# Kernel tuning notes

Measured on AMD Instinct MI355X. Metric: run time of the kernel, lower is better.

## Reference

```python
import jax, jax.numpy as jnp
import numpy as np

G = 8          # n_games
D_IN = 512     # per-game input dim (equal for all games)
H1 = 1024
H2 = 1024
A = 128        # max_actions
B = 8192       # batch rows


def setup_inputs() -> dict:
    key = jax.random.key(0)
    ks = jax.random.split(key, 9)
    state = jax.random.normal(ks[0], (B, D_IN), dtype=jnp.float32)
    idx = jax.random.randint(ks[1], (B,), 0, G, dtype=jnp.int32)
    # per-game input linears: uniform(-1/sqrt(fan_in), 1/sqrt(fan_in))
    lim1 = 1.0 / np.sqrt(D_IN)
    W1 = jax.random.uniform(ks[2], (G, D_IN, H1), minval=-lim1, maxval=lim1, dtype=jnp.float32)
    b1 = jax.random.uniform(ks[3], (G, H1), minval=-lim1, maxval=lim1, dtype=jnp.float32)
    # shared linear
    lim2 = 1.0 / np.sqrt(H1)
    W2 = jax.random.uniform(ks[4], (H1, H2), minval=-lim2, maxval=lim2, dtype=jnp.float32)
    b2 = jax.random.uniform(ks[5], (H2,), minval=-lim2, maxval=lim2, dtype=jnp.float32)
    # per-game output heads: uniform(-0.003, 0.003)
    W3 = jax.random.uniform(ks[6], (G, H2, A), minval=-0.003, maxval=0.003, dtype=jnp.float32)
    b3 = jax.random.uniform(ks[7], (G, A), minval=-0.003, maxval=0.003, dtype=jnp.float32)
    return {"state": state, "idx": idx, "W1": W1, "b1": b1, "W2": W2, "b2": b2, "W3": W3, "b3": b3}


def reference(state, idx, W1, b1, W2, b2, W3, b3):
    # Torch code concatenates per-game groups in sorted-unique-idx order,
    # i.e. a stable permutation of rows by idx; reproduce exactly.
    perm = jnp.argsort(idx, stable=True)          # [B]
    s = state[perm]                               # [B, D_IN]
    g = idx[perm]                                 # [B] game of each permuted row
    # routed first layer: compute all games then gather per-row game
    h1_all = jnp.einsum('bd,gdh->bgh', s, W1) + b1            # [B, G, H1]
    h1 = jax.nn.relu(jnp.take_along_axis(h1_all, g[:, None, None], axis=1)[:, 0, :])  # [B, H1]
    h_f = jax.nn.relu(h1 @ W2 + b2)                            # [B, H2]
    a = jnp.tanh(jnp.einsum('bh,gha->bga', h_f, W3) + b3)      # [B, G, A]
    # NOTE: original gathers heads with the ORIGINAL (unpermuted) idx,
    # even though rows of `a` are in permuted order. Reproduce faithfully.
    out = jnp.take_along_axis(a, idx[:, None, None], axis=1)[:, 0, :]  # [B, A]
    return out
```

## Files before the change

kernel.cpp:

```cpp
#include <hip/hip_runtime.h>
#include <math.h>

#define G_GAMES 8
#define D_IN 512
#define H1 1024
#define H2 1024
#define A_DIM 128
#define B_ROWS 8192

typedef short bf16x8 __attribute__((ext_vector_type(8)));
typedef float f32x4 __attribute__((ext_vector_type(4)));

#define WS_OFF   0u
#define WS_PERM  256u
#define WS_SPERM 33280u
#define WS_W1T   (WS_SPERM + B_ROWS*D_IN*2u)
#define WS_W2T   (WS_W1T + G_GAMES*D_IN*H1*2u)
#define WS_W3T   (WS_W2T + (unsigned)H1*H2*2u)
#define WS_H1    (WS_W3T + G_GAMES*H2*A_DIM*2u)
#define WS_HF    WS_SPERM

__device__ __forceinline__ unsigned short f2bf(float x) {
  union { float f; unsigned int u; } v; v.f = x;
  unsigned int r = v.u + 0x7fffu + ((v.u >> 16) & 1u);
  return (unsigned short)(r >> 16);
}

__device__ __forceinline__ void async_load16(const void* gptr, void* ldsptr) {
  __builtin_amdgcn_global_load_lds(
      (const __attribute__((address_space(1))) unsigned int*)gptr,
      (__attribute__((address_space(3))) unsigned int*)ldsptr,
      16, 0, 0);
}

__device__ void sort_256(const int* __restrict__ idx, int* __restrict__ perm,
                         int* __restrict__ off) {
  __shared__ int wtot[4][9];
  __shared__ int wbase[4][9];
  __shared__ int offs[9];
  const int t = threadIdx.x, lane = t & 63, wave = t >> 6;
  int my[32];
#pragma unroll
  for (int i = 0; i < 8; ++i) {
    const int4 a = *(const int4*)(idx + t * 32 + i * 4);
    my[i*4+0] = a.x; my[i*4+1] = a.y; my[i*4+2] = a.z; my[i*4+3] = a.w;
  }
  int local[8] = {0,0,0,0,0,0,0,0};
#pragma unroll
  for (int i = 0; i < 32; ++i) local[my[i]]++;
  int incl[8];
#pragma unroll
  for (int g = 0; g < 8; ++g) {
    int v = local[g];
#pragma unroll
    for (int d = 1; d < 64; d <<= 1) {
      const int n = __shfl_up(v, d);
      if (lane >= d) v += n;
    }
    incl[g] = v;
  }
  if (lane == 63) {
#pragma unroll
    for (int g = 0; g < 8; ++g) wtot[wave][g] = incl[g];
  }
  __syncthreads();
  if (t < 8) {
    int s = 0;
#pragma unroll
    for (int w = 0; w < 4; ++w) { wbase[w][t] = s; s += wtot[w][t]; }
    wtot[0][t] = s;
  }
  __syncthreads();
  if (t == 0) {
    int s = 0;
#pragma unroll
    for (int g = 0; g < 8; ++g) { offs[g] = s; off[g] = s; s += wtot[0][g]; }
    offs[8] = s; off[8] = s;
  }
  __syncthreads();
  int start[8];
#pragma unroll
  for (int g = 0; g < 8; ++g)
    start[g] = offs[g] + wbase[wave][g] + (incl[g] - local[g]);
#pragma unroll
  for (int i = 0; i < 32; ++i) {
    const int g = my[i];
    perm[start[g]++] = t * 32 + i;
  }
}

__device__ void trans_tile(const float* __restrict__ in,
                           unsigned short* __restrict__ out,
                           int R, int C, int xt, int yt, int z) {
  in  += (size_t)z * R * C;
  out += (size_t)z * R * C;
  __shared__ float tile[64][65];
  const int c0 = xt * 64, r0 = yt * 64;
  const int tx = threadIdx.x & 63, ty = threadIdx.x >> 6;
#pragma unroll
  for (int rr = ty; rr < 64; rr += 4)
    tile[rr][tx] = in[(size_t)(r0 + rr) * C + c0 + tx];
  __syncthreads();
#pragma unroll
  for (int cc = ty; cc < 64; cc += 4)
    out[(size_t)(c0 + cc) * R + r0 + tx] = f2bf(tile[tx][cc]);
}

__global__ __launch_bounds__(256) void k_pre1(const float* __restrict__ W1,
                                              const float* __restrict__ W2,
                                              const float* __restrict__ W3,
                                              const int* __restrict__ idx,
                                              unsigned short* __restrict__ W1T,
                                              unsigned short* __restrict__ W2T,
                                              unsigned short* __restrict__ W3T,
                                              int* __restrict__ perm,
                                              int* __restrict__ off) {
  const int b = blockIdx.x;
  if (b < 1024) {
    const int z = b >> 7, r = b & 127;
    trans_tile(W1, W1T, D_IN, H1, r & 15, r >> 4, z);
  } else if (b < 1280) {
    const int r = b - 1024;
    trans_tile(W2, W2T, H1, H2, r & 15, r >> 4, 0);
  } else if (b < 1536) {
    const int r = (b - 1280) & 31, z = (b - 1280) >> 5;
    trans_tile(W3, W3T, H2, A_DIM, r & 1, r >> 1, z);
  } else {
    sort_256(idx, perm, off);
  }
}

__global__ __launch_bounds__(256) void k_gather(const float* __restrict__ state,
                                                const int* __restrict__ perm,
                                                unsigned short* __restrict__ sPerm) {
  const int p = blockIdx.x * 2 + (threadIdx.x >> 7);
  const int c = (threadIdx.x & 127) << 2;
  const int src = perm[p];
  const float4 v = *(const float4*)(state + (size_t)src * D_IN + c);
  ushort4 o;
  o.x = f2bf(v.x); o.y = f2bf(v.y); o.z = f2bf(v.z); o.w = f2bf(v.w);
  *(ushort4*)(sPerm + (size_t)p * D_IN + c) = o;
}

template <int KTOT>
__device__ __forceinline__ void gemm_db_core(const unsigned short* const* aP,
                                             const unsigned short* const* bP,
                                             char* smem, int tid, f32x4 acc[4][4]) {
  const int lane = tid & 63, wave = tid >> 6;
  const int wm = wave & 1, wn = wave >> 1;
  const int sw = lane & 15, quad = lane >> 4;
  const int mA = wm * 64 + sw;
  const int nB = wn * 64 + sw;
  char* A0 = smem;          char* A1 = smem + 16384;
  char* B0 = smem + 32768;  char* B1 = smem + 49152;
  const int NIT = KTOT >> 6;
#pragma unroll
  for (int c = 0; c < 4; ++c) {
    async_load16(aP[c], A0 + (wave * 32 + c * 8) * 128);
    async_load16(bP[c], B0 + (wave * 32 + c * 8) * 128);
  }
#pragma unroll 2
  for (int k = 0; k < NIT; ++k) {
    __syncthreads();
    char* A = (k & 1) ? A1 : A0;
    char* B = (k & 1) ? B1 : B0;
    if (k + 1 < NIT) {
      char* An = (k & 1) ? A0 : A1;
      char* Bn = (k & 1) ? B0 : B1;
      const int koff = (k + 1) << 6;
#pragma unroll
      for (int c = 0; c < 4; ++c) {
        async_load16(aP[c] + koff, An + (wave * 32 + c * 8) * 128);
        async_load16(bP[c] + koff, Bn + (wave * 32 + c * 8) * 128);
      }
    }
#pragma unroll
    for (int ks = 0; ks < 2; ++ks) {
      const int u = ((((ks << 2) + quad) ^ (sw & 7)) << 4);
      bf16x8 aF[4], bF[4];
#pragma unroll
      for (int i = 0; i < 4; ++i) {
        aF[i] = *(const bf16x8*)(A + (mA + i * 16) * 128 + u);
        bF[i] = *(const bf16x8*)(B + (nB + i * 16) * 128 + u);
      }
#pragma unroll
      for (int i = 0; i < 4; ++i)
#pragma unroll
        for (int j = 0; j < 4; ++j)
          acc[i][j] = __builtin_amdgcn_mfma_f32_16x16x32_bf16(aF[i], bF[j], acc[i][j], 0, 0, 0);
    }
  }
}

__device__ __forceinline__ bool seg_map(const int* __restrict__ off, int T,
                                        int& g, int& seg1, int& row0) {
  int base = 0;
  for (int gg = 0; gg < 8; ++gg) {
    const int s = off[gg], e = off[gg + 1];
    const int nt = (e - s + 127) >> 7;
    if (T < base + nt) { g = gg; seg1 = e; row0 = s + (T - base) * 128; return true; }
    base += nt;
  }
  return false;
}

__device__ __forceinline__ bool seg_map32(const int* __restrict__ off, int T,
                                          int& g, int& seg1, int& row0) {
  int base = 0;
  for (int gg = 0; gg < 8; ++gg) {
    const int s = off[gg], e = off[gg + 1];
    const int nt = (e - s + 31) >> 5;
    if (T < base + nt) { g = gg; seg1 = e; row0 = s + (T - base) * 32; return true; }
    base += nt;
  }
  return false;
}

__device__ __forceinline__ void epilogue_bf16(char* smem, const f32x4 acc[4][4],
                                              const float* bj, int tid,
                                              unsigned short* __restrict__ outp,
                                              size_t ldOut, int row0, int col0,
                                              int vrows) {
  const int lane = tid & 63, wave = tid >> 6;
  const int wm = wave & 1, wn = wave >> 1;
  const int sw = lane & 15, quad = lane >> 4;
  __syncthreads();
#pragma unroll
  for (int i = 0; i < 4; ++i)
#pragma unroll
    for (int j = 0; j < 4; ++j)
#pragma unroll
      for (int r = 0; r < 4; ++r) {
        const int row = wm * 64 + i * 16 + quad * 4 + r;
        const int col = wn * 64 + j * 16 + sw;
        const float v = fmaxf(acc[i][j][r] + bj[j], 0.0f);
        *(unsigned short*)(smem + row * 264 + col * 2) = f2bf(v);
      }
  __syncthreads();
#pragma unroll
  for (int q = 0; q < 8; ++q) {
    const int idxq = q * 256 + tid;
    const int row = idxq >> 4, ch = idxq & 15;
    if (row < vrows) {
      const uint2 lo = *(const uint2*)(smem + row * 264 + ch * 16);
      const uint2 hi = *(const uint2*)(smem + row * 264 + ch * 16 + 8);
      uint4 v; v.x = lo.x; v.y = lo.y; v.z = hi.x; v.w = hi.y;
      *(uint4*)((char*)outp + ((size_t)(row0 + row) * ldOut + col0 + ch * 8) * 2) = v;
    }
  }
}

__global__ __launch_bounds__(256) void k_gemm1(const unsigned short* __restrict__ sPerm,
                                               const unsigned short* __restrict__ W1T,
                                               const float* __restrict__ b1,
                                               const int* __restrict__ off,
                                               unsigned short* __restrict__ h1out) {
  __shared__ char smem[65536];
  int g, seg1, row0;
  if (!seg_map(off, blockIdx.x, g, seg1, row0)) return;
  const int col0 = blockIdx.y * 128;
  const int tid = threadIdx.x, lane = tid & 63, wave = tid >> 6;
  const int gcol = ((lane & 7) ^ (lane >> 3)) << 3;
  const unsigned short* aP[4];
  const unsigned short* bP[4];
#pragma unroll
  for (int c = 0; c < 4; ++c) {
    const int rl = wave * 32 + c * 8 + (lane >> 3);
    int p = row0 + rl;
    if (p > seg1 - 1) p = seg1 - 1;
    aP[c] = sPerm + (size_t)p * D_IN + gcol;
    bP[c] = W1T + (size_t)g * H1 * D_IN + (size_t)(col0 + rl) * D_IN + gcol;
  }
  f32x4 acc[4][4] = {};
  gemm_db_core<D_IN>(aP, bP, smem, tid, acc);
  const int wn = wave >> 1, sw = lane & 15;
  const float* bg = b1 + g * H1;
  float bj[4];
#pragma unroll
  for (int j = 0; j < 4; ++j) bj[j] = bg[col0 + wn * 64 + j * 16 + sw];
  const int vrows = min(128, seg1 - row0);
  epilogue_bf16(smem, acc, bj, tid, h1out, H1, row0, col0, vrows);
}

__global__ __launch_bounds__(256) void k_gemm2(const unsigned short* __restrict__ h1in,
                                               const unsigned short* __restrict__ W2T,
                                               const float* __restrict__ b2,
                                               unsigned short* __restrict__ hfout) {
  __shared__ char smem[65536];
  const int row0 = blockIdx.x * 128, col0 = blockIdx.y * 128;
  const int tid = threadIdx.x, lane = tid & 63, wave = tid >> 6;
  const int gcol = ((lane & 7) ^ (lane >> 3)) << 3;
  const unsigned short* aP[4];
  const unsigned short* bP[4];
#pragma unroll
  for (int c = 0; c < 4; ++c) {
    const int rl = wave * 32 + c * 8 + (lane >> 3);
    aP[c] = h1in + (size_t)(row0 + rl) * H1 + gcol;
    bP[c] = W2T + (size_t)(col0 + rl) * H1 + gcol;
  }
  f32x4 acc[4][4] = {};
  gemm_db_core<H1>(aP, bP, smem, tid, acc);
  const int wn = wave >> 1, sw = lane & 15;
  float bj[4];
#pragma unroll
  for (int j = 0; j < 4; ++j) bj[j] = b2[col0 + wn * 64 + j * 16 + sw];
  epilogue_bf16(smem, acc, bj, tid, hfout, H2, row0, col0, 128);
}

__global__ __launch_bounds__(256) void k_gemm3(const unsigned short* __restrict__ hf,
                                               const unsigned short* __restrict__ W3T,
                                               const float* __restrict__ b3,
                                               const int* __restrict__ off,
                                               const int* __restrict__ perm,
                                               float* __restrict__ outp) {
  __shared__ char smem[40960];
  int g, seg1, row0;
  if (!seg_map32(off, blockIdx.x, g, seg1, row0)) return;
  const int tid = threadIdx.x, lane = tid & 63, wave = tid >> 6;
  const int wm = wave & 1, wn = wave >> 1;
  const int sw = lane & 15, quad = lane >> 4;
  const int gcol = ((lane & 7) ^ (lane >> 3)) << 3;
  int q0 = row0 + wave * 8 + (lane >> 3);
  if (q0 > seg1 - 1) q0 = seg1 - 1;
  const unsigned short* aP = hf + (size_t)perm[q0] * H2 + gcol;
  const unsigned short* bP[4];
#pragma unroll
  for (int c = 0; c < 4; ++c) {
    const int rl = wave * 32 + c * 8 + (lane >> 3);
    bP[c] = W3T + (size_t)g * A_DIM * H2 + (size_t)rl * H2 + gcol;
  }
  char* A0 = smem;         char* A1 = smem + 4096;
  char* B0 = smem + 8192;  char* B1 = smem + 24576;
  const int mA = wm * 16 + sw;
  const int nB = wn * 64 + sw;
  f32x4 acc[4] = {};
  async_load16(aP, A0 + (wave * 8) * 128);
#pragma unroll
  for (int c = 0; c < 4; ++c)
    async_load16(bP[c], B0 + (wave * 32 + c * 8) * 128);
#pragma unroll 2
  for (int k = 0; k < (H2 >> 6); ++k) {
    __syncthreads();
    char* A = (k & 1) ? A1 : A0;
    char* B = (k & 1) ? B1 : B0;
    if (k + 1 < (H2 >> 6)) {
      char* An = (k & 1) ? A0 : A1;
      char* Bn = (k & 1) ? B0 : B1;
      const int koff = (k + 1) << 6;
      async_load16(aP + koff, An + (wave * 8) * 128);
#pragma unroll
      for (int c = 0; c < 4; ++c)
        async_load16(bP[c] + koff, Bn + (wave * 32 + c * 8) * 128);
    }
#pragma unroll
    for (int ks = 0; ks < 2; ++ks) {
      const int u = ((((ks << 2) + quad) ^ (sw & 7)) << 4);
      const bf16x8 aF = *(const bf16x8*)(A + mA * 128 + u);
      bf16x8 bF[4];
#pragma unroll
      for (int j = 0; j < 4; ++j)
        bF[j] = *(const bf16x8*)(B + (nB + j * 16) * 128 + u);
#pragma unroll
      for (int j = 0; j < 4; ++j)
        acc[j] = __builtin_amdgcn_mfma_f32_16x16x32_bf16(aF, bF[j], acc[j], 0, 0, 0);
    }
  }
  const float* bg = b3 + g * A_DIM;
  float bj[4];
#pragma unroll
  for (int j = 0; j < 4; ++j) bj[j] = bg[wn * 64 + j * 16 + sw];
  __syncthreads();
#pragma unroll
  for (int j = 0; j < 4; ++j)
#pragma unroll
    for (int r = 0; r < 4; ++r) {
      const int row = wm * 16 + quad * 4 + r;
      const int col = wn * 64 + j * 16 + sw;
      *(float*)(smem + row * 528 + col * 4) = tanhf(acc[j][r] + bj[j]);
    }
  __syncthreads();
#pragma unroll
  for (int qq = 0; qq < 4; ++qq) {
    const int idxq = qq * 256 + tid;
    const int row = idxq >> 5, ch = idxq & 31;
    if (row0 + row < seg1) {
      const uint4 v = *(const uint4*)(smem + row * 528 + ch * 16);
      *(uint4*)((char*)outp + ((size_t)perm[row0 + row] * A_DIM + ch * 4) * 4) = v;
    }
  }
}

extern "C" void kernel_launch(void* const* d_in, const int* in_sizes, int n_in,
                              void* d_out, int out_size, void* d_ws, size_t ws_size,
                              hipStream_t stream) {
  (void)in_sizes; (void)n_in; (void)out_size; (void)ws_size;
  const float* state = (const float*)d_in[0];
  const int*   idx   = (const int*)d_in[1];
  const float* W1    = (const float*)d_in[2];
  const float* b1    = (const float*)d_in[3];
  const float* W2    = (const float*)d_in[4];
  const float* b2    = (const float*)d_in[5];
  const float* W3    = (const float*)d_in[6];
  const float* b3    = (const float*)d_in[7];
  float* outp = (float*)d_out;
  char* ws = (char*)d_ws;
  int* off  = (int*)(ws + WS_OFF);
  int* perm = (int*)(ws + WS_PERM);
  unsigned short* sPerm = (unsigned short*)(ws + WS_SPERM);
  unsigned short* W1T   = (unsigned short*)(ws + WS_W1T);
  unsigned short* W2T   = (unsigned short*)(ws + WS_W2T);
  unsigned short* W3T   = (unsigned short*)(ws + WS_W3T);
  unsigned short* h1    = (unsigned short*)(ws + WS_H1);
  unsigned short* hf    = (unsigned short*)(ws + WS_HF);

  hipLaunchKernelGGL(k_pre1, dim3(1537), dim3(256), 0, stream,
                     W1, W2, W3, idx, W1T, W2T, W3T, perm, off);
  hipLaunchKernelGGL(k_gather, dim3(B_ROWS / 2), dim3(256), 0, stream, state, perm, sPerm);
  hipLaunchKernelGGL(k_gemm1, dim3(72, 8), dim3(256), 0, stream, sPerm, W1T, b1, off, h1);
  hipLaunchKernelGGL(k_gemm2, dim3(64, 8), dim3(256), 0, stream, h1, W2T, b2, hf);
  hipLaunchKernelGGL(k_gemm3, dim3(264), dim3(256), 0, stream, hf, W3T, b3, off, perm, outp);
}
```

Before: 156.3 us.

## Fuse state gather and bf16 conversion into gemm1, vectorize weight transpose

Removes the separate gather kernel. gemm1 now reads fp32 state rows through the permutation directly, converts them to bf16 in registers, and writes them into swizzled LDS. The weight-transpose tiles switch to float4 loads with packed bf16 conversion and 16-byte stores, which cuts global store transactions. In exchange, the A-operand loads become synchronous register loads instead of async LDS loads, and they read twice the bytes per element (fp32), which may reduce overlap inside gemm1.

```diff
diff --git a/kernel.cpp b/kernel.cpp
--- a/kernel.cpp
+++ b/kernel.cpp
@@ -26,6 +26,12 @@
   return (unsigned short)(r >> 16);
 }
 
+__device__ __forceinline__ unsigned int cvt_pk_bf16(float lo, float hi) {
+  unsigned int r;
+  asm("v_cvt_pk_bf16_f32 %0, %1, %2" : "=v"(r) : "v"(lo), "v"(hi));
+  return r;
+}
+
 __device__ __forceinline__ void async_load16(const void* gptr, void* ldsptr) {
   __builtin_amdgcn_global_load_lds(
       (const __attribute__((address_space(1))) unsigned int*)gptr,
@@ -94,16 +100,33 @@
                            int R, int C, int xt, int yt, int z) {
   in  += (size_t)z * R * C;
   out += (size_t)z * R * C;
-  __shared__ float tile[64][65];
+  __shared__ unsigned short tl[64][68];
   const int c0 = xt * 64, r0 = yt * 64;
-  const int tx = threadIdx.x & 63, ty = threadIdx.x >> 6;
-#pragma unroll
-  for (int rr = ty; rr < 64; rr += 4)
-    tile[rr][tx] = in[(size_t)(r0 + rr) * C + c0 + tx];
-  __syncthreads();
-#pragma unroll
-  for (int cc = ty; cc < 64; cc += 4)
-    out[(size_t)(c0 + cc) * R + r0 + tx] = f2bf(tile[tx][cc]);
+  const int t = threadIdx.x;
+#pragma unroll
+  for (int pass = 0; pass < 4; ++pass) {
+    const int id = pass * 256 + t;
+    const int r = id >> 4, f4c = (id & 15) << 2;
+    const float4 v = *(const float4*)(in + (size_t)(r0 + r) * C + c0 + f4c);
+    uint2 w;
+    w.x = cvt_pk_bf16(v.x, v.y);
+    w.y = cvt_pk_bf16(v.z, v.w);
+    *(uint2*)&tl[r][f4c] = w;
+  }
+  __syncthreads();
+#pragma unroll
+  for (int pass = 0; pass < 2; ++pass) {
+    const int cc = t >> 2, k0 = ((t & 3) << 3) + (pass << 5);
+    unsigned short u[8];
+#pragma unroll
+    for (int j = 0; j < 8; ++j) u[j] = tl[k0 + j][cc];
+    uint4 v;
+    v.x = (unsigned)u[0] | ((unsigned)u[1] << 16);
+    v.y = (unsigned)u[2] | ((unsigned)u[3] << 16);
+    v.z = (unsigned)u[4] | ((unsigned)u[5] << 16);
+    v.w = (unsigned)u[6] | ((unsigned)u[7] << 16);
+    *(uint4*)(out + (size_t)(c0 + cc) * R + r0 + k0) = v;
+  }
 }
 
 __global__ __launch_bounds__(256) void k_pre1(const float* __restrict__ W1,
@@ -130,18 +153,6 @@
   }
 }
 
-__global__ __launch_bounds__(256) void k_gather(const float* __restrict__ state,
-                                                const int* __restrict__ perm,
-                                                unsigned short* __restrict__ sPerm) {
-  const int p = blockIdx.x * 2 + (threadIdx.x >> 7);
-  const int c = (threadIdx.x & 127) << 2;
-  const int src = perm[p];
-  const float4 v = *(const float4*)(state + (size_t)src * D_IN + c);
-  ushort4 o;
-  o.x = f2bf(v.x); o.y = f2bf(v.y); o.z = f2bf(v.z); o.w = f2bf(v.w);
-  *(ushort4*)(sPerm + (size_t)p * D_IN + c) = o;
-}
-
 template <int KTOT>
 __device__ __forceinline__ void gemm_db_core(const unsigned short* const* aP,
                                              const unsigned short* const* bP,
@@ -250,30 +261,101 @@
   }
 }
 
-__global__ __launch_bounds__(256) void k_gemm1(const unsigned short* __restrict__ sPerm,
-                                               const unsigned short* __restrict__ W1T,
-                                               const float* __restrict__ b1,
-                                               const int* __restrict__ off,
-                                               unsigned short* __restrict__ h1out) {
-  __shared__ char smem[65536];
+__global__ __launch_bounds__(256, 2) void k_gemm1(const float* __restrict__ state,
+                                                  const int* __restrict__ perm,
+                                                  const unsigned short* __restrict__ W1T,
+                                                  const float* __restrict__ b1,
+                                                  const int* __restrict__ off,
+                                                  unsigned short* __restrict__ h1out) {
+  __shared__ __align__(16) char smem[65536];
   int g, seg1, row0;
   if (!seg_map(off, blockIdx.x, g, seg1, row0)) return;
   const int col0 = blockIdx.y * 128;
   const int tid = threadIdx.x, lane = tid & 63, wave = tid >> 6;
+  const int wm = wave & 1, wn = wave >> 1;
+  const int sw = lane & 15, quad = lane >> 4;
+  const int lc = lane & 7;
   const int gcol = ((lane & 7) ^ (lane >> 3)) << 3;
-  const unsigned short* aP[4];
+  const float* aS[4];
+  int ldsA[4];
   const unsigned short* bP[4];
 #pragma unroll
   for (int c = 0; c < 4; ++c) {
     const int rl = wave * 32 + c * 8 + (lane >> 3);
     int p = row0 + rl;
     if (p > seg1 - 1) p = seg1 - 1;
-    aP[c] = sPerm + (size_t)p * D_IN + gcol;
-    bP[c] = W1T + (size_t)g * H1 * D_IN + (size_t)(col0 + rl) * D_IN + gcol;
-  }
+    aS[c]  = state + (size_t)perm[p] * D_IN + lc * 8;
+    ldsA[c] = rl * 128 + ((lc ^ (rl & 7)) << 4);
+    bP[c]  = W1T + (size_t)g * H1 * D_IN + (size_t)(col0 + rl) * D_IN + gcol;
+  }
+  char* A0 = smem;          char* A1 = smem + 16384;
+  char* B0 = smem + 32768;  char* B1 = smem + 49152;
+  const int mA = wm * 64 + sw, nB = wn * 64 + sw;
   f32x4 acc[4][4] = {};
-  gemm_db_core<D_IN>(aP, bP, smem, tid, acc);
-  const int wn = wave >> 1, sw = lane & 15;
+  {
+    float4 t0[4], t1[4];
+#pragma unroll
+    for (int c = 0; c < 4; ++c) {
+      t0[c] = *(const float4*)(aS[c]);
+      t1[c] = *(const float4*)(aS[c] + 4);
+      async_load16(bP[c], B0 + (wave * 32 + c * 8) * 128);
+    }
+#pragma unroll
+    for (int c = 0; c < 4; ++c) {
+      uint4 pk;
+      pk.x = cvt_pk_bf16(t0[c].x, t0[c].y);
+      pk.y = cvt_pk_bf16(t0[c].z, t0[c].w);
+      pk.z = cvt_pk_bf16(t1[c].x, t1[c].y);
+      pk.w = cvt_pk_bf16(t1[c].z, t1[c].w);
+      *(uint4*)(A0 + ldsA[c]) = pk;
+    }
+  }
+  const int NIT = D_IN >> 6;
+#pragma unroll 2
+  for (int k = 0; k < NIT; ++k) {
+    __syncthreads();
+    char* A = (k & 1) ? A1 : A0;
+    char* B = (k & 1) ? B1 : B0;
+    float4 t0[4], t1[4];
+    const bool pf = (k + 1 < NIT);
+    if (pf) {
+      char* Bn = (k & 1) ? B0 : B1;
+      const int koff = (k + 1) << 6;
+#pragma unroll
+      for (int c = 0; c < 4; ++c) {
+        t0[c] = *(const float4*)(aS[c] + koff);
+        t1[c] = *(const float4*)(aS[c] + koff + 4);
+        async_load16(bP[c] + koff, Bn + (wave * 32 + c * 8) * 128);
+      }
+    }
+#pragma unroll
+    for (int ks = 0; ks < 2; ++ks) {
+      const int u = ((((ks << 2) + quad) ^ (sw & 7)) << 4);
+      bf16x8 aF[4], bF[4];
+#pragma unroll
+      for (int i = 0; i < 4; ++i) {
+        aF[i] = *(const bf16x8*)(A + (mA + i * 16) * 128 + u);
+        bF[i] = *(const bf16x8*)(B + (nB + i * 16) * 128 + u);
+      }
+#pragma unroll
+      for (int i = 0; i < 4; ++i)
+#pragma unroll
+        for (int j = 0; j < 4; ++j)
+          acc[i][j] = __builtin_amdgcn_mfma_f32_16x16x32_bf16(aF[i], bF[j], acc[i][j], 0, 0, 0);
+    }
+    if (pf) {
+      char* An = (k & 1) ? A0 : A1;
+#pragma unroll
+      for (int c = 0; c < 4; ++c) {
+        uint4 pk;
+        pk.x = cvt_pk_bf16(t0[c].x, t0[c].y);
+        pk.y = cvt_pk_bf16(t0[c].z, t0[c].w);
+        pk.z = cvt_pk_bf16(t1[c].x, t1[c].y);
+        pk.w = cvt_pk_bf16(t1[c].z, t1[c].w);
+        *(uint4*)(An + ldsA[c]) = pk;
+      }
+    }
+  }
   const float* bg = b1 + g * H1;
   float bj[4];
 #pragma unroll
@@ -286,7 +368,7 @@
                                                const unsigned short* __restrict__ W2T,
                                                const float* __restrict__ b2,
                                                unsigned short* __restrict__ hfout) {
-  __shared__ char smem[65536];
+  __shared__ __align__(16) char smem[65536];
   const int row0 = blockIdx.x * 128, col0 = blockIdx.y * 128;
   const int tid = threadIdx.x, lane = tid & 63, wave = tid >> 6;
   const int gcol = ((lane & 7) ^ (lane >> 3)) << 3;
@@ -313,7 +395,7 @@
                                                const int* __restrict__ off,
                                                const int* __restrict__ perm,
                                                float* __restrict__ outp) {
-  __shared__ char smem[40960];
+  __shared__ __align__(16) char smem[40960];
   int g, seg1, row0;
   if (!seg_map32(off, blockIdx.x, g, seg1, row0)) return;
   const int tid = threadIdx.x, lane = tid & 63, wave = tid >> 6;
@@ -406,7 +488,6 @@
   char* ws = (char*)d_ws;
   int* off  = (int*)(ws + WS_OFF);
   int* perm = (int*)(ws + WS_PERM);
-  unsigned short* sPerm = (unsigned short*)(ws + WS_SPERM);
   unsigned short* W1T   = (unsigned short*)(ws + WS_W1T);
   unsigned short* W2T   = (unsigned short*)(ws + WS_W2T);
   unsigned short* W3T   = (unsigned short*)(ws + WS_W3T);
@@ -415,8 +496,8 @@
 
   hipLaunchKernelGGL(k_pre1, dim3(1537), dim3(256), 0, stream,
                      W1, W2, W3, idx, W1T, W2T, W3T, perm, off);
-  hipLaunchKernelGGL(k_gather, dim3(B_ROWS / 2), dim3(256), 0, stream, state, perm, sPerm);
-  hipLaunchKernelGGL(k_gemm1, dim3(72, 8), dim3(256), 0, stream, sPerm, W1T, b1, off, h1);
+  hipLaunchKernelGGL(k_gemm1, dim3(72, 8), dim3(256), 0, stream,
+                     state, perm, W1T, b1, off, h1);
   hipLaunchKernelGGL(k_gemm2, dim3(64, 8), dim3(256), 0, stream, h1, W2T, b2, hf);
   hipLaunchKernelGGL(k_gemm3, dim3(264), dim3(256), 0, stream, hf, W3T, b3, off, perm, outp);
 }
```

Measured after the change: 152.9 us. 1.02x faster.
